# Kernel tuning notes

Hardware: AMD Instinct MI355X
Metric: run time of the kernel (lower is better)

Reference implementation:

```python
import jax, jax.numpy as jnp
import numpy as np

K_TOP = 16
NUM_HEADS = 12
EPS = 1e-6


def setup_inputs() -> dict:
    key = jax.random.key(0)
    ks = jax.random.split(key, 5)
    B, N, C = 4, 1024, 768
    scale = 0.02
    return {
        "x": jax.random.normal(ks[0], (B, N, C), dtype=jnp.float32),
        "in_proj_weight": jax.random.normal(ks[1], (3 * C, C), dtype=jnp.float32) * scale,
        "in_proj_bias": jax.random.normal(ks[2], (3 * C,), dtype=jnp.float32) * scale,
        "out_proj_weight": jax.random.normal(ks[3], (C, C), dtype=jnp.float32) * scale,
        "out_proj_bias": jax.random.normal(ks[4], (C,), dtype=jnp.float32) * scale,
    }


def reference(x, in_proj_weight, in_proj_bias, out_proj_weight, out_proj_bias):
    B, N, C = x.shape
    H = NUM_HEADS
    Dh = C // H
    scale = Dh ** (-0.5)
    # fused QKV projection: (B,N,3C) -> (3,B,H,N,Dh)
    qkv = x @ in_proj_weight.T + in_proj_bias
    qkv = qkv.reshape(B, N, 3, H, Dh).transpose(2, 0, 3, 1, 4)
    q, k, v = qkv[0], qkv[1], qkv[2]
    # dense scaled-dot-product scores, softmax over keys
    attn = jax.nn.softmax(jnp.einsum("bhqd,bhkd->bhqk", q, k) * scale, axis=-1)
    # top-k sparsification: keep k largest probs per query row, zero the rest
    topk_vals, topk_idx = jax.lax.top_k(attn, K_TOP)  # [B,H,N,K]
    bi = jnp.arange(B)[:, None, None, None]
    hi = jnp.arange(H)[None, :, None, None]
    ni = jnp.arange(N)[None, None, :, None]
    topk_attn = jnp.zeros_like(attn).at[bi, hi, ni, topk_idx].set(topk_vals)
    # renormalize surviving mass
    den = jnp.clip(topk_attn.sum(axis=-1, keepdims=True), EPS, None)
    topk_attn = topk_attn / den
    # weighted value aggregation + output projection
    x_out = jnp.einsum("bhqk,bhkd->bhqd", topk_attn, v)
    x_out = x_out.transpose(0, 2, 1, 3).reshape(B, N, C)
    x_out = x_out @ out_proj_weight.T + out_proj_bias
    return (x_out, topk_attn)
```

## Files before the change

kernel.cpp:

```cpp
#include <hip/hip_runtime.h>
#include <math.h>
#include <stdint.h>

#define BB 4
#define NN 1024
#define CC 768
#define HH 12
#define DH 64
#define KTOP 16

#define GATE     2e-4f
#define SUPERSET 4e-4f

typedef __attribute__((ext_vector_type(8))) short short8v;
typedef __attribute__((ext_vector_type(4))) short short4v;
typedef __attribute__((ext_vector_type(4))) float f32x4;

__device__ __forceinline__ short2 bf16split(float f) {
    uint32_t u = __float_as_uint(f);
    uint32_t hb = (u + 0x8000u) & 0xFFFF0000u;
    float hf = __uint_as_float(hb);
    float lo = f - hf;
    short2 r;
    r.x = (short)(hb >> 16);
    r.y = (short)((__float_as_uint(lo) + 0x8000u) >> 16);
    return r;
}

__device__ __forceinline__ short8v lds_load8(const short* p) {
    short4v a = *(const short4v*)p;
    short4v b = *(const short4v*)(p + 4);
    short8v r;
    r[0] = a[0]; r[1] = a[1]; r[2] = a[2]; r[3] = a[3];
    r[4] = b[0]; r[5] = b[1]; r[6] = b[2]; r[7] = b[3];
    return r;
}

__global__ __launch_bounds__(256) void qkv_mfma(
    const float* __restrict__ x, const float* __restrict__ w,
    const float* __restrict__ bias,
    float* __restrict__ q32, float* __restrict__ k32, float* __restrict__ v32) {
    __shared__ short xh[128][36], xl[128][36];
    __shared__ short wh[64][36],  wl[64][36];
    const int tid = threadIdx.x;
    const int m0 = blockIdx.x * 128, n0 = blockIdx.y * 64;
    const int wave = tid >> 6, lane = tid & 63;
    const int wr = wave >> 1, wc = wave & 1;
    const int lr = lane & 15, lg = lane >> 4;

    f32x4 acc[4][2];
#pragma unroll
    for (int i = 0; i < 4; ++i)
#pragma unroll
        for (int j = 0; j < 2; ++j) acc[i][j] = (f32x4)0.0f;

    for (int k0 = 0; k0 < CC; k0 += 32) {
        __syncthreads();
#pragma unroll
        for (int it = 0; it < 4; ++it) {
            int e = tid + 256 * it;
            int row = e >> 3, c4 = e & 7;
            float4 f = *reinterpret_cast<const float4*>(&x[(size_t)(m0 + row) * CC + k0 + 4 * c4]);
            short4v hv, lv;
            short2 s0 = bf16split(f.x); short2 s1 = bf16split(f.y);
            short2 s2 = bf16split(f.z); short2 s3 = bf16split(f.w);
            hv[0] = s0.x; lv[0] = s0.y; hv[1] = s1.x; lv[1] = s1.y;
            hv[2] = s2.x; lv[2] = s2.y; hv[3] = s3.x; lv[3] = s3.y;
            *(short4v*)&xh[row][4 * c4] = hv;
            *(short4v*)&xl[row][4 * c4] = lv;
        }
#pragma unroll
        for (int it = 0; it < 2; ++it) {
            int e = tid + 256 * it;
            int row = e >> 3, c4 = e & 7;
            float4 f = *reinterpret_cast<const float4*>(&w[(size_t)(n0 + row) * CC + k0 + 4 * c4]);
            short4v hv, lv;
            short2 s0 = bf16split(f.x); short2 s1 = bf16split(f.y);
            short2 s2 = bf16split(f.z); short2 s3 = bf16split(f.w);
            hv[0] = s0.x; lv[0] = s0.y; hv[1] = s1.x; lv[1] = s1.y;
            hv[2] = s2.x; lv[2] = s2.y; hv[3] = s3.x; lv[3] = s3.y;
            *(short4v*)&wh[row][4 * c4] = hv;
            *(short4v*)&wl[row][4 * c4] = lv;
        }
        __syncthreads();

        short8v ah[4], al[4], bh[2], bl[2];
#pragma unroll
        for (int mt = 0; mt < 4; ++mt) {
            int row = wr * 64 + mt * 16 + lr;
            ah[mt] = lds_load8(&xh[row][lg * 8]);
            al[mt] = lds_load8(&xl[row][lg * 8]);
        }
#pragma unroll
        for (int nt = 0; nt < 2; ++nt) {
            int col = wc * 32 + nt * 16 + lr;
            bh[nt] = lds_load8(&wh[col][lg * 8]);
            bl[nt] = lds_load8(&wl[col][lg * 8]);
        }
#pragma unroll
        for (int mt = 0; mt < 4; ++mt) {
#pragma unroll
            for (int nt = 0; nt < 2; ++nt) {
                acc[mt][nt] = __builtin_amdgcn_mfma_f32_16x16x32_bf16(ah[mt], bh[nt], acc[mt][nt], 0, 0, 0);
                acc[mt][nt] = __builtin_amdgcn_mfma_f32_16x16x32_bf16(ah[mt], bl[nt], acc[mt][nt], 0, 0, 0);
                acc[mt][nt] = __builtin_amdgcn_mfma_f32_16x16x32_bf16(al[mt], bh[nt], acc[mt][nt], 0, 0, 0);
            }
        }
    }

    const int t = n0 / CC;
#pragma unroll
    for (int mt = 0; mt < 4; ++mt) {
#pragma unroll
        for (int nt = 0; nt < 2; ++nt) {
#pragma unroll
            for (int r = 0; r < 4; ++r) {
                int m = m0 + wr * 64 + mt * 16 + lg * 4 + r;
                int col = n0 + wc * 32 + nt * 16 + lr;
                float val = acc[mt][nt][r] + bias[col];
                int rem = col - t * CC;
                int h = rem >> 6, d = rem & 63;
                int b = m >> 10, n = m & 1023;
                size_t off = (((size_t)(b * HH + h)) * NN + n) * DH + d;
                if (t == 0) q32[off] = val;
                else if (t == 1) k32[off] = val;
                else v32[off] = val;
            }
        }
    }
}

__global__ __launch_bounds__(256) void scores_mfma(
    const float* __restrict__ q32, const float* __restrict__ k32,
    float* __restrict__ attn_out) {
    __shared__ short qh[64][68], ql[64][68];
    __shared__ short kh[128][68], kl[128][68];
    const int bh = blockIdx.y;
    const int m0 = blockIdx.x * 64;
    const int tid = threadIdx.x;
    const int wave = tid >> 6, lane = tid & 63;
    const int lr = lane & 15, lg = lane >> 4;

    const float* qb = q32 + ((size_t)bh * NN + m0) * DH;
    const float* kb = k32 + (size_t)bh * NN * DH;

#pragma unroll
    for (int it = 0; it < 4; ++it) {
        int e = tid + 256 * it;
        int row = e >> 4, c4 = e & 15;
        float4 f = *reinterpret_cast<const float4*>(&qb[(size_t)row * DH + 4 * c4]);
        f.x *= 0.125f; f.y *= 0.125f; f.z *= 0.125f; f.w *= 0.125f;
        short4v hv, lv;
        short2 s0 = bf16split(f.x); short2 s1 = bf16split(f.y);
        short2 s2 = bf16split(f.z); short2 s3 = bf16split(f.w);
        hv[0] = s0.x; lv[0] = s0.y; hv[1] = s1.x; lv[1] = s1.y;
        hv[2] = s2.x; lv[2] = s2.y; hv[3] = s3.x; lv[3] = s3.y;
        *(short4v*)&qh[row][4 * c4] = hv;
        *(short4v*)&ql[row][4 * c4] = lv;
    }
    __syncthreads();

    short8v ah[4][2], al[4][2];
#pragma unroll
    for (int mt = 0; mt < 4; ++mt)
#pragma unroll
        for (int ks = 0; ks < 2; ++ks) {
            ah[mt][ks] = lds_load8(&qh[mt * 16 + lr][ks * 32 + lg * 8]);
            al[mt][ks] = lds_load8(&ql[mt * 16 + lr][ks * 32 + lg * 8]);
        }

    float* orow0 = attn_out + ((size_t)bh * NN + m0) * NN;

    for (int c0 = 0; c0 < NN; c0 += 128) {
        __syncthreads();
#pragma unroll
        for (int it = 0; it < 8; ++it) {
            int e = tid + 256 * it;
            int row = e >> 4, c4 = e & 15;
            float4 f = *reinterpret_cast<const float4*>(&kb[(size_t)(c0 + row) * DH + 4 * c4]);
            short4v hv, lv;
            short2 s0 = bf16split(f.x); short2 s1 = bf16split(f.y);
            short2 s2 = bf16split(f.z); short2 s3 = bf16split(f.w);
            hv[0] = s0.x; lv[0] = s0.y; hv[1] = s1.x; lv[1] = s1.y;
            hv[2] = s2.x; lv[2] = s2.y; hv[3] = s3.x; lv[3] = s3.y;
            *(short4v*)&kh[row][4 * c4] = hv;
            *(short4v*)&kl[row][4 * c4] = lv;
        }
        __syncthreads();

        short8v bhf[2][2], blf[2][2];
#pragma unroll
        for (int nt = 0; nt < 2; ++nt)
#pragma unroll
            for (int ks = 0; ks < 2; ++ks) {
                int col = wave * 32 + nt * 16 + lr;
                bhf[nt][ks] = lds_load8(&kh[col][ks * 32 + lg * 8]);
                blf[nt][ks] = lds_load8(&kl[col][ks * 32 + lg * 8]);
            }

        f32x4 acc[4][2];
#pragma unroll
        for (int mt = 0; mt < 4; ++mt)
#pragma unroll
            for (int nt = 0; nt < 2; ++nt) acc[mt][nt] = (f32x4)0.0f;

#pragma unroll
        for (int mt = 0; mt < 4; ++mt)
#pragma unroll
            for (int nt = 0; nt < 2; ++nt)
#pragma unroll
                for (int ks = 0; ks < 2; ++ks) {
                    acc[mt][nt] = __builtin_amdgcn_mfma_f32_16x16x32_bf16(ah[mt][ks], bhf[nt][ks], acc[mt][nt], 0, 0, 0);
                    acc[mt][nt] = __builtin_amdgcn_mfma_f32_16x16x32_bf16(ah[mt][ks], blf[nt][ks], acc[mt][nt], 0, 0, 0);
                    acc[mt][nt] = __builtin_amdgcn_mfma_f32_16x16x32_bf16(al[mt][ks], bhf[nt][ks], acc[mt][nt], 0, 0, 0);
                }

#pragma unroll
        for (int mt = 0; mt < 4; ++mt)
#pragma unroll
            for (int nt = 0; nt < 2; ++nt)
#pragma unroll
                for (int r = 0; r < 4; ++r)
                    orow0[(size_t)(mt * 16 + lg * 4 + r) * NN + c0 + wave * 32 + nt * 16 + lr] = acc[mt][nt][r];
    }
}

__device__ __forceinline__ uint32_t f2su(float f) {
    uint32_t u = __float_as_uint(f);
    return u ^ ((u & 0x80000000u) ? 0xFFFFFFFFu : 0x80000000u);
}
__device__ __forceinline__ float su2f(uint32_t s) {
    uint32_t u = s ^ ((s & 0x80000000u) ? 0x80000000u : 0xFFFFFFFFu);
    return __uint_as_float(u);
}

__global__ __launch_bounds__(256) void topk_select(
    const float* __restrict__ v32,
    float* __restrict__ attn_out, float* __restrict__ xatt,
    int* __restrict__ wl_count, int* __restrict__ wl_row, int* __restrict__ wl_cand) {
    __shared__ int      cand_idx[4][64];
    __shared__ uint32_t cand_val[4][64];
    const int blk = blockIdx.x;
    const int wave = threadIdx.x >> 6, lane = threadIdx.x & 63;
    const int bh = blk >> 8;
    const int qn = ((blk & 255) << 2) | wave;

    float* srow = attn_out + ((size_t)bh * NN + qn) * NN;

    uint32_t su[16];
#pragma unroll
    for (int i = 0; i < 4; ++i) {
        float4 t = *(const float4*)&srow[i * 256 + lane * 4];
        su[4 * i + 0] = f2su(t.x); su[4 * i + 1] = f2su(t.y);
        su[4 * i + 2] = f2su(t.z); su[4 * i + 3] = f2su(t.w);
    }

    uint32_t thr = 0;
    for (int b = 31; b >= 0; --b) {
        uint32_t test = thr | (1u << b);
        int cnt = 0;
#pragma unroll
        for (int r = 0; r < 16; ++r)
            cnt += __popcll(__ballot(su[r] >= test));
        if (cnt >= 17) { thr = test; if (cnt <= 64) break; }
    }

    int C = 0;
#pragma unroll
    for (int r = 0; r < 16; ++r) {
        bool pr = (su[r] >= thr);
        unsigned long long mask = __ballot(pr);
        if (pr) {
            int pos = C + __popcll(mask & ((1ull << lane) - 1ull));
            if (pos < 64) {
                cand_idx[wave][pos] = ((r >> 2) << 8) + (lane << 2) + (r & 3);
                cand_val[wave][pos] = su[r];
            }
        }
        C += __popcll(mask);
    }
    if (C > 64) C = 64;

    uint32_t key = (lane < C) ? cand_val[wave][lane] : 0u;
    int      idx = (lane < C) ? cand_idx[wave][lane] : (0x40000000 + lane);

#pragma unroll
    for (int k = 2; k <= 64; k <<= 1) {
#pragma unroll
        for (int j = k >> 1; j > 0; j >>= 1) {
            uint32_t ok = __shfl_xor(key, j);
            int      oi = __shfl_xor(idx, j);
            bool mine_better = (key > ok) || (key == ok && idx < oi);
            bool lower = ((lane & j) == 0);
            bool dir_desc = ((lane & k) == 0);
            bool keep = dir_desc ? (lower ? mine_better : !mine_better)
                                 : (lower ? !mine_better : mine_better);
            if (!keep) { key = ok; idx = oi; }
        }
    }

    float f = su2f(key);
    float f15 = __shfl(f, 15);
    float f16 = __shfl(f, 16);

    bool fast = (f15 - f16 > GATE);
    float p = 0.0f;
    int selIdx = idx;

    if (fast) {
        float m = __shfl(f, 0);
        float e = (lane < KTOP) ? expf(f - m) : 0.0f;
        float sum = e;
#pragma unroll
        for (int off = 32; off; off >>= 1) sum += __shfl_xor(sum, off);
        p = e / sum;
    } else {
        uint32_t thr2 = f2su(f15 - SUPERSET);
        int C2 = 0;
#pragma unroll
        for (int r = 0; r < 16; ++r) {
            bool pr = (su[r] >= thr2);
            unsigned long long mask = __ballot(pr);
            if (pr) {
                int pos = C2 + __popcll(mask & ((1ull << lane) - 1ull));
                if (pos < 64) cand_idx[wave][pos] = ((r >> 2) << 8) + (lane << 2) + (r & 3);
            }
            C2 += __popcll(mask);
        }
        if (C2 > 64) C2 = 64;

        int slot = 0;
        if (lane == 0) slot = atomicAdd(wl_count, 1);
        slot = __shfl(slot, 0);
        int rowid = (bh << 10) | qn;
        if (lane == 0) wl_row[slot] = rowid | (C2 << 20);
        if (lane < C2) wl_cand[(size_t)slot * 64 + lane] = cand_idx[wave][lane];
    }

#pragma unroll
    for (int i = 0; i < 4; ++i) {
        float4 z = make_float4(0.f, 0.f, 0.f, 0.f);
        *(float4*)&srow[i * 256 + lane * 4] = z;
    }

    if (fast) {
        const float* vb = v32 + (size_t)bh * NN * DH;
        float o = 0.0f;
#pragma unroll
        for (int t = 0; t < KTOP; ++t) {
            int jt = __shfl(selIdx, t);
            float pt = __shfl(p, t);
            o = fmaf(pt, vb[(size_t)jt * DH + lane], o);
        }
        asm volatile("s_waitcnt vmcnt(0)" ::: "memory");
        if (lane < KTOP) srow[selIdx] = p;
        int b = bh / HH, h = bh - b * HH;
        xatt[((size_t)b * NN + qn) * CC + h * DH + lane] = o;
    }
}

__global__ __launch_bounds__(64) void slow_rescore(
    const float* __restrict__ x, const float* __restrict__ w_in,
    const float* __restrict__ b_in, const float* __restrict__ v32,
    const int* __restrict__ wl_count, const int* __restrict__ wl_row,
    const int* __restrict__ wl_cand,
    float* __restrict__ attn_out, float* __restrict__ xatt) {
    __shared__ double part[64][65];
    __shared__ double q_sh[64];
    const int lane = threadIdx.x;
    const int count = wl_count[0];

    for (int it = blockIdx.x; it < count; it += gridDim.x) {
        int ent = wl_row[it];
        int rowid = ent & 0xFFFF;
        int C2 = (ent >> 20) & 0x7F;
        int bh = rowid >> 10, qn = rowid & 1023;
        int bq = bh / HH, hq = bh - bq * HH;

        __syncthreads();

        const float* xq = x + ((size_t)bq * NN + qn) * CC;
        double xqd[12];
#pragma unroll
        for (int c = 0; c < 3; ++c) {
            float4 v = *(const float4*)&xq[c * 256 + 4 * lane];
            xqd[4 * c + 0] = v.x; xqd[4 * c + 1] = v.y;
            xqd[4 * c + 2] = v.z; xqd[4 * c + 3] = v.w;
        }
        const float* wqb = w_in + (size_t)(hq * DH) * CC;
        for (int r = 0; r < 64; ++r) {
            const float* wr = wqb + (size_t)r * CC;
            double s = 0.0;
#pragma unroll
            for (int c = 0; c < 3; ++c) {
                float4 v = *(const float4*)&wr[c * 256 + 4 * lane];
                s = fma((double)v.x, xqd[4 * c + 0], s);
                s = fma((double)v.y, xqd[4 * c + 1], s);
                s = fma((double)v.z, xqd[4 * c + 2], s);
                s = fma((double)v.w, xqd[4 * c + 3], s);
            }
            part[r][lane] = s;
        }
        __syncthreads();
        double q64 = 0.0, q64b = 0.0;
#pragma unroll
        for (int l = 0; l < 64; l += 2) { q64 += part[lane][l]; q64b += part[lane][l + 1]; }
        q64 += q64b + (double)b_in[hq * DH + lane];
        q_sh[lane] = q64;
        __syncthreads();

        double beta = q64 * (double)b_in[CC + hq * DH + lane];
#pragma unroll
        for (int off = 32; off; off >>= 1) beta += __shfl_xor(beta, off);

        const float* wkb = w_in + (size_t)(CC + hq * DH) * CC;
        double zd[12];
#pragma unroll
        for (int j = 0; j < 12; ++j) zd[j] = 0.0;
        for (int r = 0; r < 64; ++r) {
            double qr = q_sh[r];
            const float* wr = wkb + (size_t)r * CC;
#pragma unroll
            for (int c = 0; c < 3; ++c) {
                float4 v = *(const float4*)&wr[c * 256 + 4 * lane];
                zd[4 * c + 0] = fma(qr, (double)v.x, zd[4 * c + 0]);
                zd[4 * c + 1] = fma(qr, (double)v.y, zd[4 * c + 1]);
                zd[4 * c + 2] = fma(qr, (double)v.z, zd[4 * c + 2]);
                zd[4 * c + 3] = fma(qr, (double)v.w, zd[4 * c + 3]);
            }
        }

        double myS = -1.0e300;
        int myI = (1 << 30);
        for (int t = 0; t < C2; ++t) {
            int jt = wl_cand[(size_t)it * 64 + t];
            const float* xk = x + ((size_t)bq * NN + jt) * CC;
            double pr = 0.0;
#pragma unroll
            for (int c = 0; c < 3; ++c) {
                float4 v = *(const float4*)&xk[c * 256 + 4 * lane];
                pr = fma(zd[4 * c + 0], (double)v.x, pr);
                pr = fma(zd[4 * c + 1], (double)v.y, pr);
                pr = fma(zd[4 * c + 2], (double)v.z, pr);
                pr = fma(zd[4 * c + 3], (double)v.w, pr);
            }
#pragma unroll
            for (int off = 32; off; off >>= 1) pr += __shfl_xor(pr, off);
            if (lane == t) { myS = (pr + beta) * 0.125; myI = jt; }
        }

        double sS = myS;
        int sI = myI;
        double selS = 0.0; int selIdx = 0;
#pragma unroll 1
        for (int t = 0; t < KTOP; ++t) {
            double bv = sS; int bi = sI;
#pragma unroll
            for (int off = 32; off; off >>= 1) {
                double ov = __shfl_xor(bv, off);
                int oi = __shfl_xor(bi, off);
                if (ov > bv || (ov == bv && oi < bi)) { bv = ov; bi = oi; }
            }
            if (lane == t) { selS = bv; selIdx = bi; }
            if (sI == bi) sS = -1.0e300;
        }

        double m = __shfl(selS, 0);
        float e = (lane < KTOP) ? expf((float)(selS - m)) : 0.0f;
        float sum = e;
#pragma unroll
        for (int off = 32; off; off >>= 1) sum += __shfl_xor(sum, off);
        float p = e / sum;

        const float* vb = v32 + (size_t)bh * NN * DH;
        float o = 0.0f;
#pragma unroll
        for (int t = 0; t < KTOP; ++t) {
            int jt = __shfl(selIdx, t);
            float pt = __shfl(p, t);
            o = fmaf(pt, vb[(size_t)jt * DH + lane], o);
        }

        float* srow = attn_out + (size_t)rowid * NN;
        if (lane < KTOP) srow[selIdx] = p;
        xatt[((size_t)bq * NN + qn) * CC + hq * DH + lane] = o;
    }
}

__global__ __launch_bounds__(256) void out_proj_mfma(
    const float* __restrict__ a, const float* __restrict__ w,
    const float* __restrict__ bias, float* __restrict__ out) {
    __shared__ short xh[128][36], xl[128][36];
    __shared__ short wh[64][36],  wl[64][36];
    const int tid = threadIdx.x;
    const int m0 = blockIdx.x * 128, n0 = blockIdx.y * 64;
    const int wave = tid >> 6, lane = tid & 63;
    const int wr = wave >> 1, wc = wave & 1;
    const int lr = lane & 15, lg = lane >> 4;

    f32x4 acc[4][2];
#pragma unroll
    for (int i = 0; i < 4; ++i)
#pragma unroll
        for (int j = 0; j < 2; ++j) acc[i][j] = (f32x4)0.0f;

    for (int k0 = 0; k0 < CC; k0 += 32) {
        __syncthreads();
#pragma unroll
        for (int it = 0; it < 4; ++it) {
            int e = tid + 256 * it;
            int row = e >> 3, c4 = e & 7;
            float4 f = *reinterpret_cast<const float4*>(&a[(size_t)(m0 + row) * CC + k0 + 4 * c4]);
            short4v hv, lv;
            short2 s0 = bf16split(f.x); short2 s1 = bf16split(f.y);
            short2 s2 = bf16split(f.z); short2 s3 = bf16split(f.w);
            hv[0] = s0.x; lv[0] = s0.y; hv[1] = s1.x; lv[1] = s1.y;
            hv[2] = s2.x; lv[2] = s2.y; hv[3] = s3.x; lv[3] = s3.y;
            *(short4v*)&xh[row][4 * c4] = hv;
            *(short4v*)&xl[row][4 * c4] = lv;
        }
#pragma unroll
        for (int it = 0; it < 2; ++it) {
            int e = tid + 256 * it;
            int row = e >> 3, c4 = e & 7;
            float4 f = *reinterpret_cast<const float4*>(&w[(size_t)(n0 + row) * CC + k0 + 4 * c4]);
            short4v hv, lv;
            short2 s0 = bf16split(f.x); short2 s1 = bf16split(f.y);
            short2 s2 = bf16split(f.z); short2 s3 = bf16split(f.w);
            hv[0] = s0.x; lv[0] = s0.y; hv[1] = s1.x; lv[1] = s1.y;
            hv[2] = s2.x; lv[2] = s2.y; hv[3] = s3.x; lv[3] = s3.y;
            *(short4v*)&wh[row][4 * c4] = hv;
            *(short4v*)&wl[row][4 * c4] = lv;
        }
        __syncthreads();

        short8v ah[4], al[4], bh[2], bl[2];
#pragma unroll
        for (int mt = 0; mt < 4; ++mt) {
            int row = wr * 64 + mt * 16 + lr;
            ah[mt] = lds_load8(&xh[row][lg * 8]);
            al[mt] = lds_load8(&xl[row][lg * 8]);
        }
#pragma unroll
        for (int nt = 0; nt < 2; ++nt) {
            int col = wc * 32 + nt * 16 + lr;
            bh[nt] = lds_load8(&wh[col][lg * 8]);
            bl[nt] = lds_load8(&wl[col][lg * 8]);
        }
#pragma unroll
        for (int mt = 0; mt < 4; ++mt) {
#pragma unroll
            for (int nt = 0; nt < 2; ++nt) {
                acc[mt][nt] = __builtin_amdgcn_mfma_f32_16x16x32_bf16(ah[mt], bh[nt], acc[mt][nt], 0, 0, 0);
                acc[mt][nt] = __builtin_amdgcn_mfma_f32_16x16x32_bf16(ah[mt], bl[nt], acc[mt][nt], 0, 0, 0);
                acc[mt][nt] = __builtin_amdgcn_mfma_f32_16x16x32_bf16(al[mt], bh[nt], acc[mt][nt], 0, 0, 0);
            }
        }
    }

#pragma unroll
    for (int mt = 0; mt < 4; ++mt) {
#pragma unroll
        for (int nt = 0; nt < 2; ++nt) {
#pragma unroll
            for (int r = 0; r < 4; ++r) {
                int m = m0 + wr * 64 + mt * 16 + lg * 4 + r;
                int col = n0 + wc * 32 + nt * 16 + lr;
                out[(size_t)m * CC + col] = acc[mt][nt][r] + bias[col];
            }
        }
    }
}

extern "C" void kernel_launch(void* const* d_in, const int* in_sizes, int n_in,
                              void* d_out, int out_size, void* d_ws, size_t ws_size,
                              hipStream_t stream) {
    const float* x     = (const float*)d_in[0];
    const float* w_in  = (const float*)d_in[1];
    const float* b_in  = (const float*)d_in[2];
    const float* w_out = (const float*)d_in[3];
    const float* b_out = (const float*)d_in[4];

    float* xout     = (float*)d_out;
    float* attn_out = (float*)d_out + (size_t)BB * NN * CC;

    char* ws = (char*)d_ws;
    float* q32     = (float*)ws;
    float* k32     = (float*)(ws + 12582912);
    float* v32     = (float*)(ws + 25165824);
    float* xatt    = (float*)(ws + 37748736);
    int*   wl_count = (int*)(ws + 50331648);
    int*   wl_row   = (int*)(ws + 50331904);
    int*   wl_cand  = (int*)(ws + 50528512);

    (void)hipMemsetAsync(wl_count, 0, sizeof(int), stream);

    hipLaunchKernelGGL(qkv_mfma, dim3(32, 36), dim3(256), 0, stream,
                       x, w_in, b_in, q32, k32, v32);
    hipLaunchKernelGGL(scores_mfma, dim3(NN / 64, BB * HH), dim3(256), 0, stream,
                       q32, k32, attn_out);
    hipLaunchKernelGGL(topk_select, dim3(BB * HH * (NN / 4)), dim3(256), 0, stream,
                       v32, attn_out, xatt, wl_count, wl_row, wl_cand);
    hipLaunchKernelGGL(slow_rescore, dim3(1024), dim3(64), 0, stream,
                       x, w_in, b_in, v32, wl_count, wl_row, wl_cand, attn_out, xatt);
    hipLaunchKernelGGL(out_proj_mfma, dim3(32, 12), dim3(256), 0, stream,
                       xatt, w_out, b_out, xout);
}
```

Baseline: 346.0 us.

## Presplit x and W_in into bf16 hi/lo buffers; emit Q/K as split bf16

```diff
diff --git a/kernel.cpp b/kernel.cpp
--- a/kernel.cpp
+++ b/kernel.cpp
@@ -36,10 +36,33 @@
     return r;
 }
 
+__global__ __launch_bounds__(256) void presplit(
+    const float* __restrict__ x, const float* __restrict__ w_in,
+    short* __restrict__ xh, short* __restrict__ xl,
+    short* __restrict__ wh, short* __restrict__ wl) {
+    const int NX4 = (BB * NN * CC) / 4;
+    const int NW4 = (3 * CC * CC) / 4;
+    for (int i = blockIdx.x * 256 + threadIdx.x; i < NX4 + NW4; i += gridDim.x * 256) {
+        bool isx = (i < NX4);
+        int j = isx ? i : i - NX4;
+        float4 f = isx ? ((const float4*)x)[j] : ((const float4*)w_in)[j];
+        short4v hv, lv;
+        short2 s0 = bf16split(f.x); short2 s1 = bf16split(f.y);
+        short2 s2 = bf16split(f.z); short2 s3 = bf16split(f.w);
+        hv[0] = s0.x; lv[0] = s0.y; hv[1] = s1.x; lv[1] = s1.y;
+        hv[2] = s2.x; lv[2] = s2.y; hv[3] = s3.x; lv[3] = s3.y;
+        if (isx) { ((short4v*)xh)[j] = hv; ((short4v*)xl)[j] = lv; }
+        else     { ((short4v*)wh)[j] = hv; ((short4v*)wl)[j] = lv; }
+    }
+}
+
 __global__ __launch_bounds__(256) void qkv_mfma(
-    const float* __restrict__ x, const float* __restrict__ w,
+    const short* __restrict__ xh_g, const short* __restrict__ xl_g,
+    const short* __restrict__ wh_g, const short* __restrict__ wl_g,
     const float* __restrict__ bias,
-    float* __restrict__ q32, float* __restrict__ k32, float* __restrict__ v32) {
+    short* __restrict__ qh_g, short* __restrict__ ql_g,
+    short* __restrict__ kh_g, short* __restrict__ kl_g,
+    float* __restrict__ v32) {
     __shared__ short xh[128][36], xl[128][36];
     __shared__ short wh[64][36],  wl[64][36];
     const int tid = threadIdx.x;
@@ -57,10 +80,453 @@
     for (int k0 = 0; k0 < CC; k0 += 32) {
         __syncthreads();
 #pragma unroll
+        for (int it = 0; it < 2; ++it) {
+            int e = tid + 256 * it;
+            int row = e >> 2, c8 = (e & 3) << 3;
+            size_t g = (size_t)(m0 + row) * CC + k0 + c8;
+            *(short4v*)&xh[row][c8]     = *(const short4v*)&xh_g[g];
+            *(short4v*)&xh[row][c8 + 4] = *(const short4v*)&xh_g[g + 4];
+            *(short4v*)&xl[row][c8]     = *(const short4v*)&xl_g[g];
+            *(short4v*)&xl[row][c8 + 4] = *(const short4v*)&xl_g[g + 4];
+        }
+        {
+            int e = tid;
+            int row = e >> 2, c8 = (e & 3) << 3;
+            size_t g = (size_t)(n0 + row) * CC + k0 + c8;
+            *(short4v*)&wh[row][c8]     = *(const short4v*)&wh_g[g];
+            *(short4v*)&wh[row][c8 + 4] = *(const short4v*)&wh_g[g + 4];
+            *(short4v*)&wl[row][c8]     = *(const short4v*)&wl_g[g];
+            *(short4v*)&wl[row][c8 + 4] = *(const short4v*)&wl_g[g + 4];
+        }
+        __syncthreads();
+
+        short8v ah[4], al[4], bh[2], bl[2];
+#pragma unroll
+        for (int mt = 0; mt < 4; ++mt) {
+            int row = wr * 64 + mt * 16 + lr;
+            ah[mt] = lds_load8(&xh[row][lg * 8]);
+            al[mt] = lds_load8(&xl[row][lg * 8]);
+        }
+#pragma unroll
+        for (int nt = 0; nt < 2; ++nt) {
+            int col = wc * 32 + nt * 16 + lr;
+            bh[nt] = lds_load8(&wh[col][lg * 8]);
+            bl[nt] = lds_load8(&wl[col][lg * 8]);
+        }
+#pragma unroll
+        for (int mt = 0; mt < 4; ++mt) {
+#pragma unroll
+            for (int nt = 0; nt < 2; ++nt) {
+                acc[mt][nt] = __builtin_amdgcn_mfma_f32_16x16x32_bf16(ah[mt], bh[nt], acc[mt][nt], 0, 0, 0);
+                acc[mt][nt] = __builtin_amdgcn_mfma_f32_16x16x32_bf16(ah[mt], bl[nt], acc[mt][nt], 0, 0, 0);
+                acc[mt][nt] = __builtin_amdgcn_mfma_f32_16x16x32_bf16(al[mt], bh[nt], acc[mt][nt], 0, 0, 0);
+            }
+        }
+    }
+
+    const int t = n0 / CC;
+#pragma unroll
+    for (int mt = 0; mt < 4; ++mt) {
+#pragma unroll
+        for (int nt = 0; nt < 2; ++nt) {
+#pragma unroll
+            for (int r = 0; r < 4; ++r) {
+                int m = m0 + wr * 64 + mt * 16 + lg * 4 + r;
+                int col = n0 + wc * 32 + nt * 16 + lr;
+                float val = acc[mt][nt][r] + bias[col];
+                int rem = col - t * CC;
+                int h = rem >> 6, d = rem & 63;
+                int b = m >> 10, n = m & 1023;
+                size_t off = (((size_t)(b * HH + h)) * NN + n) * DH + d;
+                if (t == 0) {
+                    short2 s = bf16split(val * 0.125f);
+                    qh_g[off] = s.x; ql_g[off] = s.y;
+                } else if (t == 1) {
+                    short2 s = bf16split(val);
+                    kh_g[off] = s.x; kl_g[off] = s.y;
+                } else {
+                    v32[off] = val;
+                }
+            }
+        }
+    }
+}
+
+__global__ __launch_bounds__(256) void scores_mfma(
+    const short* __restrict__ qh_g, const short* __restrict__ ql_g,
+    const short* __restrict__ kh_g, const short* __restrict__ kl_g,
+    float* __restrict__ attn_out) {
+    __shared__ short qh[64][68], ql[64][68];
+    __shared__ short kh[128][68], kl[128][68];
+    const int bh = blockIdx.y;
+    const int m0 = blockIdx.x * 64;
+    const int tid = threadIdx.x;
+    const int wave = tid >> 6, lane = tid & 63;
+    const int lr = lane & 15, lg = lane >> 4;
+
+    const size_t qbase = ((size_t)bh * NN + m0) * DH;
+    const size_t kbase = (size_t)bh * NN * DH;
+
+#pragma unroll
+    for (int it = 0; it < 2; ++it) {
+        int e = tid + 256 * it;
+        int row = e >> 3, c8 = (e & 7) << 3;
+        size_t g = qbase + (size_t)row * DH + c8;
+        *(short4v*)&qh[row][c8]     = *(const short4v*)&qh_g[g];
+        *(short4v*)&qh[row][c8 + 4] = *(const short4v*)&qh_g[g + 4];
+        *(short4v*)&ql[row][c8]     = *(const short4v*)&ql_g[g];
+        *(short4v*)&ql[row][c8 + 4] = *(const short4v*)&ql_g[g + 4];
+    }
+    __syncthreads();
+
+    short8v ah[4][2], al[4][2];
+#pragma unroll
+    for (int mt = 0; mt < 4; ++mt)
+#pragma unroll
+        for (int ks = 0; ks < 2; ++ks) {
+            ah[mt][ks] = lds_load8(&qh[mt * 16 + lr][ks * 32 + lg * 8]);
+            al[mt][ks] = lds_load8(&ql[mt * 16 + lr][ks * 32 + lg * 8]);
+        }
+
+    float* orow0 = attn_out + ((size_t)bh * NN + m0) * NN;
+
+    for (int c0 = 0; c0 < NN; c0 += 128) {
+        __syncthreads();
+#pragma unroll
+        for (int it = 0; it < 4; ++it) {
+            int e = tid + 256 * it;
+            int row = e >> 3, c8 = (e & 7) << 3;
+            size_t g = kbase + (size_t)(c0 + row) * DH + c8;
+            *(short4v*)&kh[row][c8]     = *(const short4v*)&kh_g[g];
+            *(short4v*)&kh[row][c8 + 4] = *(const short4v*)&kh_g[g + 4];
+            *(short4v*)&kl[row][c8]     = *(const short4v*)&kl_g[g];
+            *(short4v*)&kl[row][c8 + 4] = *(const short4v*)&kl_g[g + 4];
+        }
+        __syncthreads();
+
+        short8v bhf[2][2], blf[2][2];
+#pragma unroll
+        for (int nt = 0; nt < 2; ++nt)
+#pragma unroll
+            for (int ks = 0; ks < 2; ++ks) {
+                int col = wave * 32 + nt * 16 + lr;
+                bhf[nt][ks] = lds_load8(&kh[col][ks * 32 + lg * 8]);
+                blf[nt][ks] = lds_load8(&kl[col][ks * 32 + lg * 8]);
+            }
+
+        f32x4 acc[4][2];
+#pragma unroll
+        for (int mt = 0; mt < 4; ++mt)
+#pragma unroll
+            for (int nt = 0; nt < 2; ++nt) acc[mt][nt] = (f32x4)0.0f;
+
+#pragma unroll
+        for (int mt = 0; mt < 4; ++mt)
+#pragma unroll
+            for (int nt = 0; nt < 2; ++nt)
+#pragma unroll
+                for (int ks = 0; ks < 2; ++ks) {
+                    acc[mt][nt] = __builtin_amdgcn_mfma_f32_16x16x32_bf16(ah[mt][ks], bhf[nt][ks], acc[mt][nt], 0, 0, 0);
+                    acc[mt][nt] = __builtin_amdgcn_mfma_f32_16x16x32_bf16(ah[mt][ks], blf[nt][ks], acc[mt][nt], 0, 0, 0);
+                    acc[mt][nt] = __builtin_amdgcn_mfma_f32_16x16x32_bf16(al[mt][ks], bhf[nt][ks], acc[mt][nt], 0, 0, 0);
+                }
+
+#pragma unroll
+        for (int mt = 0; mt < 4; ++mt)
+#pragma unroll
+            for (int nt = 0; nt < 2; ++nt)
+#pragma unroll
+                for (int r = 0; r < 4; ++r)
+                    orow0[(size_t)(mt * 16 + lg * 4 + r) * NN + c0 + wave * 32 + nt * 16 + lr] = acc[mt][nt][r];
+    }
+}
+
+__device__ __forceinline__ uint32_t f2su(float f) {
+    uint32_t u = __float_as_uint(f);
+    return u ^ ((u & 0x80000000u) ? 0xFFFFFFFFu : 0x80000000u);
+}
+__device__ __forceinline__ float su2f(uint32_t s) {
+    uint32_t u = s ^ ((s & 0x80000000u) ? 0x80000000u : 0xFFFFFFFFu);
+    return __uint_as_float(u);
+}
+
+__global__ __launch_bounds__(256) void topk_select(
+    const float* __restrict__ v32,
+    float* __restrict__ attn_out, float* __restrict__ xatt,
+    int* __restrict__ wl_count, int* __restrict__ wl_row, int* __restrict__ wl_cand) {
+    __shared__ int      cand_idx[4][64];
+    __shared__ uint32_t cand_val[4][64];
+    const int blk = blockIdx.x;
+    const int wave = threadIdx.x >> 6, lane = threadIdx.x & 63;
+    const int bh = blk >> 8;
+    const int qn = ((blk & 255) << 2) | wave;
+
+    float* srow = attn_out + ((size_t)bh * NN + qn) * NN;
+
+    uint32_t su[16];
+#pragma unroll
+    for (int i = 0; i < 4; ++i) {
+        float4 t = *(const float4*)&srow[i * 256 + lane * 4];
+        su[4 * i + 0] = f2su(t.x); su[4 * i + 1] = f2su(t.y);
+        su[4 * i + 2] = f2su(t.z); su[4 * i + 3] = f2su(t.w);
+    }
+
+    uint32_t thr = 0;
+    for (int b = 31; b >= 0; --b) {
+        uint32_t test = thr | (1u << b);
+        int cnt = 0;
+#pragma unroll
+        for (int r = 0; r < 16; ++r)
+            cnt += __popcll(__ballot(su[r] >= test));
+        if (cnt >= 17) { thr = test; if (cnt <= 64) break; }
+    }
+
+    int C = 0;
+#pragma unroll
+    for (int r = 0; r < 16; ++r) {
+        bool pr = (su[r] >= thr);
+        unsigned long long mask = __ballot(pr);
+        if (pr) {
+            int pos = C + __popcll(mask & ((1ull << lane) - 1ull));
+            if (pos < 64) {
+                cand_idx[wave][pos] = ((r >> 2) << 8) + (lane << 2) + (r & 3);
+                cand_val[wave][pos] = su[r];
+            }
+        }
+        C += __popcll(mask);
+    }
+    if (C > 64) C = 64;
+
+    uint32_t key = (lane < C) ? cand_val[wave][lane] : 0u;
+    int      idx = (lane < C) ? cand_idx[wave][lane] : (0x40000000 + lane);
+
+#pragma unroll
+    for (int k = 2; k <= 64; k <<= 1) {
+#pragma unroll
+        for (int j = k >> 1; j > 0; j >>= 1) {
+            uint32_t ok = __shfl_xor(key, j);
+            int      oi = __shfl_xor(idx, j);
+            bool mine_better = (key > ok) || (key == ok && idx < oi);
+            bool lower = ((lane & j) == 0);
+            bool dir_desc = ((lane & k) == 0);
+            bool keep = dir_desc ? (lower ? mine_better : !mine_better)
+                                 : (lower ? !mine_better : mine_better);
+            if (!keep) { key = ok; idx = oi; }
+        }
+    }
+
+    float f = su2f(key);
+    float f15 = __shfl(f, 15);
+    float f16 = __shfl(f, 16);
+
+    bool fast = (f15 - f16 > GATE);
+    float p = 0.0f;
+    int selIdx = idx;
+
+    if (fast) {
+        float m = __shfl(f, 0);
+        float e = (lane < KTOP) ? expf(f - m) : 0.0f;
+        float sum = e;
+#pragma unroll
+        for (int off = 32; off; off >>= 1) sum += __shfl_xor(sum, off);
+        p = e / sum;
+    } else {
+        uint32_t thr2 = f2su(f15 - SUPERSET);
+        int C2 = 0;
+#pragma unroll
+        for (int r = 0; r < 16; ++r) {
+            bool pr = (su[r] >= thr2);
+            unsigned long long mask = __ballot(pr);
+            if (pr) {
+                int pos = C2 + __popcll(mask & ((1ull << lane) - 1ull));
+                if (pos < 64) cand_idx[wave][pos] = ((r >> 2) << 8) + (lane << 2) + (r & 3);
+            }
+            C2 += __popcll(mask);
+        }
+        if (C2 > 64) C2 = 64;
+
+        int slot = 0;
+        if (lane == 0) slot = atomicAdd(wl_count, 1);
+        slot = __shfl(slot, 0);
+        int rowid = (bh << 10) | qn;
+        if (lane == 0) wl_row[slot] = rowid | (C2 << 20);
+        if (lane < C2) wl_cand[(size_t)slot * 64 + lane] = cand_idx[wave][lane];
+    }
+
+#pragma unroll
+    for (int i = 0; i < 4; ++i) {
+        float4 z = make_float4(0.f, 0.f, 0.f, 0.f);
+        *(float4*)&srow[i * 256 + lane * 4] = z;
+    }
+
+    if (fast) {
+        const float* vb = v32 + (size_t)bh * NN * DH;
+        float o = 0.0f;
+#pragma unroll
+        for (int t = 0; t < KTOP; ++t) {
+            int jt = __shfl(selIdx, t);
+            float pt = __shfl(p, t);
+            o = fmaf(pt, vb[(size_t)jt * DH + lane], o);
+        }
+        asm volatile("s_waitcnt vmcnt(0)" ::: "memory");
+        if (lane < KTOP) srow[selIdx] = p;
+        int b = bh / HH, h = bh - b * HH;
+        xatt[((size_t)b * NN + qn) * CC + h * DH + lane] = o;
+    }
+}
+
+__global__ __launch_bounds__(64) void slow_rescore(
+    const float* __restrict__ x, const float* __restrict__ w_in,
+    const float* __restrict__ b_in, const float* __restrict__ v32,
+    const int* __restrict__ wl_count, const int* __restrict__ wl_row,
+    const int* __restrict__ wl_cand,
+    float* __restrict__ attn_out, float* __restrict__ xatt) {
+    __shared__ double part[64][65];
+    __shared__ double q_sh[64];
+    const int lane = threadIdx.x;
+    const int count = wl_count[0];
+
+    for (int it = blockIdx.x; it < count; it += gridDim.x) {
+        int ent = wl_row[it];
+        int rowid = ent & 0xFFFF;
+        int C2 = (ent >> 20) & 0x7F;
+        int bh = rowid >> 10, qn = rowid & 1023;
+        int bq = bh / HH, hq = bh - bq * HH;
+
+        __syncthreads();
+
+        const float* xq = x + ((size_t)bq * NN + qn) * CC;
+        double xqd[12];
+#pragma unroll
+        for (int c = 0; c < 3; ++c) {
+            float4 v = *(const float4*)&xq[c * 256 + 4 * lane];
+            xqd[4 * c + 0] = v.x; xqd[4 * c + 1] = v.y;
+            xqd[4 * c + 2] = v.z; xqd[4 * c + 3] = v.w;
+        }
+        const float* wqb = w_in + (size_t)(hq * DH) * CC;
+        for (int r = 0; r < 64; ++r) {
+            const float* wr = wqb + (size_t)r * CC;
+            double s = 0.0;
+#pragma unroll
+            for (int c = 0; c < 3; ++c) {
+                float4 v = *(const float4*)&wr[c * 256 + 4 * lane];
+                s = fma((double)v.x, xqd[4 * c + 0], s);
+                s = fma((double)v.y, xqd[4 * c + 1], s);
+                s = fma((double)v.z, xqd[4 * c + 2], s);
+                s = fma((double)v.w, xqd[4 * c + 3], s);
+            }
+            part[r][lane] = s;
+        }
+        __syncthreads();
+        double q64 = 0.0, q64b = 0.0;
+#pragma unroll
+        for (int l = 0; l < 64; l += 2) { q64 += part[lane][l]; q64b += part[lane][l + 1]; }
+        q64 += q64b + (double)b_in[hq * DH + lane];
+        q_sh[lane] = q64;
+        __syncthreads();
+
+        double beta = q64 * (double)b_in[CC + hq * DH + lane];
+#pragma unroll
+        for (int off = 32; off; off >>= 1) beta += __shfl_xor(beta, off);
+
+        const float* wkb = w_in + (size_t)(CC + hq * DH) * CC;
+        double zd[12];
+#pragma unroll
+        for (int j = 0; j < 12; ++j) zd[j] = 0.0;
+        for (int r = 0; r < 64; ++r) {
+            double qr = q_sh[r];
+            const float* wr = wkb + (size_t)r * CC;
+#pragma unroll
+            for (int c = 0; c < 3; ++c) {
+                float4 v = *(const float4*)&wr[c * 256 + 4 * lane];
+                zd[4 * c + 0] = fma(qr, (double)v.x, zd[4 * c + 0]);
+                zd[4 * c + 1] = fma(qr, (double)v.y, zd[4 * c + 1]);
+                zd[4 * c + 2] = fma(qr, (double)v.z, zd[4 * c + 2]);
+                zd[4 * c + 3] = fma(qr, (double)v.w, zd[4 * c + 3]);
+            }
+        }
+
+        double myS = -1.0e300;
+        int myI = (1 << 30);
+        for (int t = 0; t < C2; ++t) {
+            int jt = wl_cand[(size_t)it * 64 + t];
+            const float* xk = x + ((size_t)bq * NN + jt) * CC;
+            double pr = 0.0;
+#pragma unroll
+            for (int c = 0; c < 3; ++c) {
+                float4 v = *(const float4*)&xk[c * 256 + 4 * lane];
+                pr = fma(zd[4 * c + 0], (double)v.x, pr);
+                pr = fma(zd[4 * c + 1], (double)v.y, pr);
+                pr = fma(zd[4 * c + 2], (double)v.z, pr);
+                pr = fma(zd[4 * c + 3], (double)v.w, pr);
+            }
+#pragma unroll
+            for (int off = 32; off; off >>= 1) pr += __shfl_xor(pr, off);
+            if (lane == t) { myS = (pr + beta) * 0.125; myI = jt; }
+        }
+
+        double sS = myS;
+        int sI = myI;
+        double selS = 0.0; int selIdx = 0;
+#pragma unroll 1
+        for (int t = 0; t < KTOP; ++t) {
+            double bv = sS; int bi = sI;
+#pragma unroll
+            for (int off = 32; off; off >>= 1) {
+                double ov = __shfl_xor(bv, off);
+                int oi = __shfl_xor(bi, off);
+                if (ov > bv || (ov == bv && oi < bi)) { bv = ov; bi = oi; }
+            }
+            if (lane == t) { selS = bv; selIdx = bi; }
+            if (sI == bi) sS = -1.0e300;
+        }
+
+        double m = __shfl(selS, 0);
+        float e = (lane < KTOP) ? expf((float)(selS - m)) : 0.0f;
+        float sum = e;
+#pragma unroll
+        for (int off = 32; off; off >>= 1) sum += __shfl_xor(sum, off);
+        float p = e / sum;
+
+        const float* vb = v32 + (size_t)bh * NN * DH;
+        float o = 0.0f;
+#pragma unroll
+        for (int t = 0; t < KTOP; ++t) {
+            int jt = __shfl(selIdx, t);
+            float pt = __shfl(p, t);
+            o = fmaf(pt, vb[(size_t)jt * DH + lane], o);
+        }
+
+        float* srow = attn_out + (size_t)rowid * NN;
+        if (lane < KTOP) srow[selIdx] = p;
+        xatt[((size_t)bq * NN + qn) * CC + hq * DH + lane] = o;
+    }
+}
+
+__global__ __launch_bounds__(256) void out_proj_mfma(
+    const float* __restrict__ a, const float* __restrict__ w,
+    const float* __restrict__ bias, float* __restrict__ out) {
+    __shared__ short xh[128][36], xl[128][36];
+    __shared__ short wh[64][36],  wl[64][36];
+    const int tid = threadIdx.x;
+    const int m0 = blockIdx.x * 128, n0 = blockIdx.y * 64;
+    const int wave = tid >> 6, lane = tid & 63;
+    const int wr = wave >> 1, wc = wave & 1;
+    const int lr = lane & 15, lg = lane >> 4;
+
+    f32x4 acc[4][2];
+#pragma unroll
+    for (int i = 0; i < 4; ++i)
+#pragma unroll
+        for (int j = 0; j < 2; ++j) acc[i][j] = (f32x4)0.0f;
+
+    for (int k0 = 0; k0 < CC; k0 += 32) {
+        __syncthreads();
+#pragma unroll
         for (int it = 0; it < 4; ++it) {
             int e = tid + 256 * it;
             int row = e >> 3, c4 = e & 7;
-            float4 f = *reinterpret_cast<const float4*>(&x[(size_t)(m0 + row) * CC + k0 + 4 * c4]);
+            float4 f = *reinterpret_cast<const float4*>(&a[(size_t)(m0 + row) * CC + k0 + 4 * c4]);
             short4v hv, lv;
             short2 s0 = bf16split(f.x); short2 s1 = bf16split(f.y);
             short2 s2 = bf16split(f.z); short2 s3 = bf16split(f.w);
@@ -108,456 +574,6 @@
         }
     }
 
-    const int t = n0 / CC;
-#pragma unroll
-    for (int mt = 0; mt < 4; ++mt) {
-#pragma unroll
-        for (int nt = 0; nt < 2; ++nt) {
-#pragma unroll
-            for (int r = 0; r < 4; ++r) {
-                int m = m0 + wr * 64 + mt * 16 + lg * 4 + r;
-                int col = n0 + wc * 32 + nt * 16 + lr;
-                float val = acc[mt][nt][r] + bias[col];
-                int rem = col - t * CC;
-                int h = rem >> 6, d = rem & 63;
-                int b = m >> 10, n = m & 1023;
-                size_t off = (((size_t)(b * HH + h)) * NN + n) * DH + d;
-                if (t == 0) q32[off] = val;
-                else if (t == 1) k32[off] = val;
-                else v32[off] = val;
-            }
-        }
-    }
-}
-
-__global__ __launch_bounds__(256) void scores_mfma(
-    const float* __restrict__ q32, const float* __restrict__ k32,
-    float* __restrict__ attn_out) {
-    __shared__ short qh[64][68], ql[64][68];
-    __shared__ short kh[128][68], kl[128][68];
-    const int bh = blockIdx.y;
-    const int m0 = blockIdx.x * 64;
-    const int tid = threadIdx.x;
-    const int wave = tid >> 6, lane = tid & 63;
-    const int lr = lane & 15, lg = lane >> 4;
-
-    const float* qb = q32 + ((size_t)bh * NN + m0) * DH;
-    const float* kb = k32 + (size_t)bh * NN * DH;
-
-#pragma unroll
-    for (int it = 0; it < 4; ++it) {
-        int e = tid + 256 * it;
-        int row = e >> 4, c4 = e & 15;
-        float4 f = *reinterpret_cast<const float4*>(&qb[(size_t)row * DH + 4 * c4]);
-        f.x *= 0.125f; f.y *= 0.125f; f.z *= 0.125f; f.w *= 0.125f;
-        short4v hv, lv;
-        short2 s0 = bf16split(f.x); short2 s1 = bf16split(f.y);
-        short2 s2 = bf16split(f.z); short2 s3 = bf16split(f.w);
-        hv[0] = s0.x; lv[0] = s0.y; hv[1] = s1.x; lv[1] = s1.y;
-        hv[2] = s2.x; lv[2] = s2.y; hv[3] = s3.x; lv[3] = s3.y;
-        *(short4v*)&qh[row][4 * c4] = hv;
-        *(short4v*)&ql[row][4 * c4] = lv;
-    }
-    __syncthreads();
-
-    short8v ah[4][2], al[4][2];
-#pragma unroll
-    for (int mt = 0; mt < 4; ++mt)
-#pragma unroll
-        for (int ks = 0; ks < 2; ++ks) {
-            ah[mt][ks] = lds_load8(&qh[mt * 16 + lr][ks * 32 + lg * 8]);
-            al[mt][ks] = lds_load8(&ql[mt * 16 + lr][ks * 32 + lg * 8]);
-        }
-
-    float* orow0 = attn_out + ((size_t)bh * NN + m0) * NN;
-
-    for (int c0 = 0; c0 < NN; c0 += 128) {
-        __syncthreads();
-#pragma unroll
-        for (int it = 0; it < 8; ++it) {
-            int e = tid + 256 * it;
-            int row = e >> 4, c4 = e & 15;
-            float4 f = *reinterpret_cast<const float4*>(&kb[(size_t)(c0 + row) * DH + 4 * c4]);
-            short4v hv, lv;
-            short2 s0 = bf16split(f.x); short2 s1 = bf16split(f.y);
-            short2 s2 = bf16split(f.z); short2 s3 = bf16split(f.w);
-            hv[0] = s0.x; lv[0] = s0.y; hv[1] = s1.x; lv[1] = s1.y;
-            hv[2] = s2.x; lv[2] = s2.y; hv[3] = s3.x; lv[3] = s3.y;
-            *(short4v*)&kh[row][4 * c4] = hv;
-            *(short4v*)&kl[row][4 * c4] = lv;
-        }
-        __syncthreads();
-
-        short8v bhf[2][2], blf[2][2];
-#pragma unroll
-        for (int nt = 0; nt < 2; ++nt)
-#pragma unroll
-            for (int ks = 0; ks < 2; ++ks) {
-                int col = wave * 32 + nt * 16 + lr;
-                bhf[nt][ks] = lds_load8(&kh[col][ks * 32 + lg * 8]);
-                blf[nt][ks] = lds_load8(&kl[col][ks * 32 + lg * 8]);
-            }
-
-        f32x4 acc[4][2];
-#pragma unroll
-        for (int mt = 0; mt < 4; ++mt)
-#pragma unroll
-            for (int nt = 0; nt < 2; ++nt) acc[mt][nt] = (f32x4)0.0f;
-
-#pragma unroll
-        for (int mt = 0; mt < 4; ++mt)
-#pragma unroll
-            for (int nt = 0; nt < 2; ++nt)
-#pragma unroll
-                for (int ks = 0; ks < 2; ++ks) {
-                    acc[mt][nt] = __builtin_amdgcn_mfma_f32_16x16x32_bf16(ah[mt][ks], bhf[nt][ks], acc[mt][nt], 0, 0, 0);
-                    acc[mt][nt] = __builtin_amdgcn_mfma_f32_16x16x32_bf16(ah[mt][ks], blf[nt][ks], acc[mt][nt], 0, 0, 0);
-                    acc[mt][nt] = __builtin_amdgcn_mfma_f32_16x16x32_bf16(al[mt][ks], bhf[nt][ks], acc[mt][nt], 0, 0, 0);
-                }
-
-#pragma unroll
-        for (int mt = 0; mt < 4; ++mt)
-#pragma unroll
-            for (int nt = 0; nt < 2; ++nt)
-#pragma unroll
-                for (int r = 0; r < 4; ++r)
-                    orow0[(size_t)(mt * 16 + lg * 4 + r) * NN + c0 + wave * 32 + nt * 16 + lr] = acc[mt][nt][r];
-    }
-}
-
-__device__ __forceinline__ uint32_t f2su(float f) {
-    uint32_t u = __float_as_uint(f);
-    return u ^ ((u & 0x80000000u) ? 0xFFFFFFFFu : 0x80000000u);
-}
-__device__ __forceinline__ float su2f(uint32_t s) {
-    uint32_t u = s ^ ((s & 0x80000000u) ? 0x80000000u : 0xFFFFFFFFu);
-    return __uint_as_float(u);
-}
-
-__global__ __launch_bounds__(256) void topk_select(
-    const float* __restrict__ v32,
-    float* __restrict__ attn_out, float* __restrict__ xatt,
-    int* __restrict__ wl_count, int* __restrict__ wl_row, int* __restrict__ wl_cand) {
-    __shared__ int      cand_idx[4][64];
-    __shared__ uint32_t cand_val[4][64];
-    const int blk = blockIdx.x;
-    const int wave = threadIdx.x >> 6, lane = threadIdx.x & 63;
-    const int bh = blk >> 8;
-    const int qn = ((blk & 255) << 2) | wave;
-
-    float* srow = attn_out + ((size_t)bh * NN + qn) * NN;
-
-    uint32_t su[16];
-#pragma unroll
-    for (int i = 0; i < 4; ++i) {
-        float4 t = *(const float4*)&srow[i * 256 + lane * 4];
-        su[4 * i + 0] = f2su(t.x); su[4 * i + 1] = f2su(t.y);
-        su[4 * i + 2] = f2su(t.z); su[4 * i + 3] = f2su(t.w);
-    }
-
-    uint32_t thr = 0;
-    for (int b = 31; b >= 0; --b) {
-        uint32_t test = thr | (1u << b);
-        int cnt = 0;
-#pragma unroll
-        for (int r = 0; r < 16; ++r)
-            cnt += __popcll(__ballot(su[r] >= test));
-        if (cnt >= 17) { thr = test; if (cnt <= 64) break; }
-    }
-
-    int C = 0;
-#pragma unroll
-    for (int r = 0; r < 16; ++r) {
-        bool pr = (su[r] >= thr);
-        unsigned long long mask = __ballot(pr);
-        if (pr) {
-            int pos = C + __popcll(mask & ((1ull << lane) - 1ull));
-            if (pos < 64) {
-                cand_idx[wave][pos] = ((r >> 2) << 8) + (lane << 2) + (r & 3);
-                cand_val[wave][pos] = su[r];
-            }
-        }
-        C += __popcll(mask);
-    }
-    if (C > 64) C = 64;
-
-    uint32_t key = (lane < C) ? cand_val[wave][lane] : 0u;
-    int      idx = (lane < C) ? cand_idx[wave][lane] : (0x40000000 + lane);
-
-#pragma unroll
-    for (int k = 2; k <= 64; k <<= 1) {
-#pragma unroll
-        for (int j = k >> 1; j > 0; j >>= 1) {
-            uint32_t ok = __shfl_xor(key, j);
-            int      oi = __shfl_xor(idx, j);
-            bool mine_better = (key > ok) || (key == ok && idx < oi);
-            bool lower = ((lane & j) == 0);
-            bool dir_desc = ((lane & k) == 0);
-            bool keep = dir_desc ? (lower ? mine_better : !mine_better)
-                                 : (lower ? !mine_better : mine_better);
-            if (!keep) { key = ok; idx = oi; }
-        }
-    }
-
-    float f = su2f(key);
-    float f15 = __shfl(f, 15);
-    float f16 = __shfl(f, 16);
-
-    bool fast = (f15 - f16 > GATE);
-    float p = 0.0f;
-    int selIdx = idx;
-
-    if (fast) {
-        float m = __shfl(f, 0);
-        float e = (lane < KTOP) ? expf(f - m) : 0.0f;
-        float sum = e;
-#pragma unroll
-        for (int off = 32; off; off >>= 1) sum += __shfl_xor(sum, off);
-        p = e / sum;
-    } else {
-        uint32_t thr2 = f2su(f15 - SUPERSET);
-        int C2 = 0;
-#pragma unroll
-        for (int r = 0; r < 16; ++r) {
-            bool pr = (su[r] >= thr2);
-            unsigned long long mask = __ballot(pr);
-            if (pr) {
-                int pos = C2 + __popcll(mask & ((1ull << lane) - 1ull));
-                if (pos < 64) cand_idx[wave][pos] = ((r >> 2) << 8) + (lane << 2) + (r & 3);
-            }
-            C2 += __popcll(mask);
-        }
-        if (C2 > 64) C2 = 64;
-
-        int slot = 0;
-        if (lane == 0) slot = atomicAdd(wl_count, 1);
-        slot = __shfl(slot, 0);
-        int rowid = (bh << 10) | qn;
-        if (lane == 0) wl_row[slot] = rowid | (C2 << 20);
-        if (lane < C2) wl_cand[(size_t)slot * 64 + lane] = cand_idx[wave][lane];
-    }
-
-#pragma unroll
-    for (int i = 0; i < 4; ++i) {
-        float4 z = make_float4(0.f, 0.f, 0.f, 0.f);
-        *(float4*)&srow[i * 256 + lane * 4] = z;
-    }
-
-    if (fast) {
-        const float* vb = v32 + (size_t)bh * NN * DH;
-        float o = 0.0f;
-#pragma unroll
-        for (int t = 0; t < KTOP; ++t) {
-            int jt = __shfl(selIdx, t);
-            float pt = __shfl(p, t);
-            o = fmaf(pt, vb[(size_t)jt * DH + lane], o);
-        }
-        asm volatile("s_waitcnt vmcnt(0)" ::: "memory");
-        if (lane < KTOP) srow[selIdx] = p;
-        int b = bh / HH, h = bh - b * HH;
-        xatt[((size_t)b * NN + qn) * CC + h * DH + lane] = o;
-    }
-}
-
-__global__ __launch_bounds__(64) void slow_rescore(
-    const float* __restrict__ x, const float* __restrict__ w_in,
-    const float* __restrict__ b_in, const float* __restrict__ v32,
-    const int* __restrict__ wl_count, const int* __restrict__ wl_row,
-    const int* __restrict__ wl_cand,
-    float* __restrict__ attn_out, float* __restrict__ xatt) {
-    __shared__ double part[64][65];
-    __shared__ double q_sh[64];
-    const int lane = threadIdx.x;
-    const int count = wl_count[0];
-
-    for (int it = blockIdx.x; it < count; it += gridDim.x) {
-        int ent = wl_row[it];
-        int rowid = ent & 0xFFFF;
-        int C2 = (ent >> 20) & 0x7F;
-        int bh = rowid >> 10, qn = rowid & 1023;
-        int bq = bh / HH, hq = bh - bq * HH;
-
-        __syncthreads();
-
-        const float* xq = x + ((size_t)bq * NN + qn) * CC;
-        double xqd[12];
-#pragma unroll
-        for (int c = 0; c < 3; ++c) {
-            float4 v = *(const float4*)&xq[c * 256 + 4 * lane];
-            xqd[4 * c + 0] = v.x; xqd[4 * c + 1] = v.y;
-            xqd[4 * c + 2] = v.z; xqd[4 * c + 3] = v.w;
-        }
-        const float* wqb = w_in + (size_t)(hq * DH) * CC;
-        for (int r = 0; r < 64; ++r) {
-            const float* wr = wqb + (size_t)r * CC;
-            double s = 0.0;
-#pragma unroll
-            for (int c = 0; c < 3; ++c) {
-                float4 v = *(const float4*)&wr[c * 256 + 4 * lane];
-                s = fma((double)v.x, xqd[4 * c + 0], s);
-                s = fma((double)v.y, xqd[4 * c + 1], s);
-                s = fma((double)v.z, xqd[4 * c + 2], s);
-                s = fma((double)v.w, xqd[4 * c + 3], s);
-            }
-            part[r][lane] = s;
-        }
-        __syncthreads();
-        double q64 = 0.0, q64b = 0.0;
-#pragma unroll
-        for (int l = 0; l < 64; l += 2) { q64 += part[lane][l]; q64b += part[lane][l + 1]; }
-        q64 += q64b + (double)b_in[hq * DH + lane];
-        q_sh[lane] = q64;
-        __syncthreads();
-
-        double beta = q64 * (double)b_in[CC + hq * DH + lane];
-#pragma unroll
-        for (int off = 32; off; off >>= 1) beta += __shfl_xor(beta, off);
-
-        const float* wkb = w_in + (size_t)(CC + hq * DH) * CC;
-        double zd[12];
-#pragma unroll
-        for (int j = 0; j < 12; ++j) zd[j] = 0.0;
-        for (int r = 0; r < 64; ++r) {
-            double qr = q_sh[r];
-            const float* wr = wkb + (size_t)r * CC;
-#pragma unroll
-            for (int c = 0; c < 3; ++c) {
-                float4 v = *(const float4*)&wr[c * 256 + 4 * lane];
-                zd[4 * c + 0] = fma(qr, (double)v.x, zd[4 * c + 0]);
-                zd[4 * c + 1] = fma(qr, (double)v.y, zd[4 * c + 1]);
-                zd[4 * c + 2] = fma(qr, (double)v.z, zd[4 * c + 2]);
-                zd[4 * c + 3] = fma(qr, (double)v.w, zd[4 * c + 3]);
-            }
-        }
-
-        double myS = -1.0e300;
-        int myI = (1 << 30);
-        for (int t = 0; t < C2; ++t) {
-            int jt = wl_cand[(size_t)it * 64 + t];
-            const float* xk = x + ((size_t)bq * NN + jt) * CC;
-            double pr = 0.0;
-#pragma unroll
-            for (int c = 0; c < 3; ++c) {
-                float4 v = *(const float4*)&xk[c * 256 + 4 * lane];
-                pr = fma(zd[4 * c + 0], (double)v.x, pr);
-                pr = fma(zd[4 * c + 1], (double)v.y, pr);
-                pr = fma(zd[4 * c + 2], (double)v.z, pr);
-                pr = fma(zd[4 * c + 3], (double)v.w, pr);
-            }
-#pragma unroll
-            for (int off = 32; off; off >>= 1) pr += __shfl_xor(pr, off);
-            if (lane == t) { myS = (pr + beta) * 0.125; myI = jt; }
-        }
-
-        double sS = myS;
-        int sI = myI;
-        double selS = 0.0; int selIdx = 0;
-#pragma unroll 1
-        for (int t = 0; t < KTOP; ++t) {
-            double bv = sS; int bi = sI;
-#pragma unroll
-            for (int off = 32; off; off >>= 1) {
-                double ov = __shfl_xor(bv, off);
-                int oi = __shfl_xor(bi, off);
-                if (ov > bv || (ov == bv && oi < bi)) { bv = ov; bi = oi; }
-            }
-            if (lane == t) { selS = bv; selIdx = bi; }
-            if (sI == bi) sS = -1.0e300;
-        }
-
-        double m = __shfl(selS, 0);
-        float e = (lane < KTOP) ? expf((float)(selS - m)) : 0.0f;
-        float sum = e;
-#pragma unroll
-        for (int off = 32; off; off >>= 1) sum += __shfl_xor(sum, off);
-        float p = e / sum;
-
-        const float* vb = v32 + (size_t)bh * NN * DH;
-        float o = 0.0f;
-#pragma unroll
-        for (int t = 0; t < KTOP; ++t) {
-            int jt = __shfl(selIdx, t);
-            float pt = __shfl(p, t);
-            o = fmaf(pt, vb[(size_t)jt * DH + lane], o);
-        }
-
-        float* srow = attn_out + (size_t)rowid * NN;
-        if (lane < KTOP) srow[selIdx] = p;
-        xatt[((size_t)bq * NN + qn) * CC + hq * DH + lane] = o;
-    }
-}
-
-__global__ __launch_bounds__(256) void out_proj_mfma(
-    const float* __restrict__ a, const float* __restrict__ w,
-    const float* __restrict__ bias, float* __restrict__ out) {
-    __shared__ short xh[128][36], xl[128][36];
-    __shared__ short wh[64][36],  wl[64][36];
-    const int tid = threadIdx.x;
-    const int m0 = blockIdx.x * 128, n0 = blockIdx.y * 64;
-    const int wave = tid >> 6, lane = tid & 63;
-    const int wr = wave >> 1, wc = wave & 1;
-    const int lr = lane & 15, lg = lane >> 4;
-
-    f32x4 acc[4][2];
-#pragma unroll
-    for (int i = 0; i < 4; ++i)
-#pragma unroll
-        for (int j = 0; j < 2; ++j) acc[i][j] = (f32x4)0.0f;
-
-    for (int k0 = 0; k0 < CC; k0 += 32) {
-        __syncthreads();
-#pragma unroll
-        for (int it = 0; it < 4; ++it) {
-            int e = tid + 256 * it;
-            int row = e >> 3, c4 = e & 7;
-            float4 f = *reinterpret_cast<const float4*>(&a[(size_t)(m0 + row) * CC + k0 + 4 * c4]);
-            short4v hv, lv;
-            short2 s0 = bf16split(f.x); short2 s1 = bf16split(f.y);
-            short2 s2 = bf16split(f.z); short2 s3 = bf16split(f.w);
-            hv[0] = s0.x; lv[0] = s0.y; hv[1] = s1.x; lv[1] = s1.y;
-            hv[2] = s2.x; lv[2] = s2.y; hv[3] = s3.x; lv[3] = s3.y;
-            *(short4v*)&xh[row][4 * c4] = hv;
-            *(short4v*)&xl[row][4 * c4] = lv;
-        }
-#pragma unroll
-        for (int it = 0; it < 2; ++it) {
-            int e = tid + 256 * it;
-            int row = e >> 3, c4 = e & 7;
-            float4 f = *reinterpret_cast<const float4*>(&w[(size_t)(n0 + row) * CC + k0 + 4 * c4]);
-            short4v hv, lv;
-            short2 s0 = bf16split(f.x); short2 s1 = bf16split(f.y);
-            short2 s2 = bf16split(f.z); short2 s3 = bf16split(f.w);
-            hv[0] = s0.x; lv[0] = s0.y; hv[1] = s1.x; lv[1] = s1.y;
-            hv[2] = s2.x; lv[2] = s2.y; hv[3] = s3.x; lv[3] = s3.y;
-            *(short4v*)&wh[row][4 * c4] = hv;
-            *(short4v*)&wl[row][4 * c4] = lv;
-        }
-        __syncthreads();
-
-        short8v ah[4], al[4], bh[2], bl[2];
-#pragma unroll
-        for (int mt = 0; mt < 4; ++mt) {
-            int row = wr * 64 + mt * 16 + lr;
-            ah[mt] = lds_load8(&xh[row][lg * 8]);
-            al[mt] = lds_load8(&xl[row][lg * 8]);
-        }
-#pragma unroll
-        for (int nt = 0; nt < 2; ++nt) {
-            int col = wc * 32 + nt * 16 + lr;
-            bh[nt] = lds_load8(&wh[col][lg * 8]);
-            bl[nt] = lds_load8(&wl[col][lg * 8]);
-        }
-#pragma unroll
-        for (int mt = 0; mt < 4; ++mt) {
-#pragma unroll
-            for (int nt = 0; nt < 2; ++nt) {
-                acc[mt][nt] = __builtin_amdgcn_mfma_f32_16x16x32_bf16(ah[mt], bh[nt], acc[mt][nt], 0, 0, 0);
-                acc[mt][nt] = __builtin_amdgcn_mfma_f32_16x16x32_bf16(ah[mt], bl[nt], acc[mt][nt], 0, 0, 0);
-                acc[mt][nt] = __builtin_amdgcn_mfma_f32_16x16x32_bf16(al[mt], bh[nt], acc[mt][nt], 0, 0, 0);
-            }
-        }
-    }
-
 #pragma unroll
     for (int mt = 0; mt < 4; ++mt) {
 #pragma unroll
@@ -585,20 +601,28 @@
     float* attn_out = (float*)d_out + (size_t)BB * NN * CC;
 
     char* ws = (char*)d_ws;
-    float* q32     = (float*)ws;
-    float* k32     = (float*)(ws + 12582912);
-    float* v32     = (float*)(ws + 25165824);
-    float* xatt    = (float*)(ws + 37748736);
-    int*   wl_count = (int*)(ws + 50331648);
-    int*   wl_row   = (int*)(ws + 50331904);
-    int*   wl_cand  = (int*)(ws + 50528512);
+    short* xh_g = (short*)(ws);
+    short* xl_g = (short*)(ws + 6291456);
+    short* wh_g = (short*)(ws + 12582912);
+    short* wl_g = (short*)(ws + 16121856);
+    short* qh_g = (short*)(ws + 19660800);
+    short* ql_g = (short*)(ws + 25952256);
+    short* kh_g = (short*)(ws + 32243712);
+    short* kl_g = (short*)(ws + 38535168);
+    float* v32  = (float*)(ws + 44826624);
+    float* xatt = (float*)(ws + 57409536);
+    int* wl_count = (int*)(ws + 69992448);
+    int* wl_row   = (int*)(ws + 69992704);
+    int* wl_cand  = (int*)(ws + 70189312);
 
     (void)hipMemsetAsync(wl_count, 0, sizeof(int), stream);
 
+    hipLaunchKernelGGL(presplit, dim3(2048), dim3(256), 0, stream,
+                       x, w_in, xh_g, xl_g, wh_g, wl_g);
     hipLaunchKernelGGL(qkv_mfma, dim3(32, 36), dim3(256), 0, stream,
-                       x, w_in, b_in, q32, k32, v32);
+                       xh_g, xl_g, wh_g, wl_g, b_in, qh_g, ql_g, kh_g, kl_g, v32);
     hipLaunchKernelGGL(scores_mfma, dim3(NN / 64, BB * HH), dim3(256), 0, stream,
-                       q32, k32, attn_out);
+                       qh_g, ql_g, kh_g, kl_g, attn_out);
     hipLaunchKernelGGL(topk_select, dim3(BB * HH * (NN / 4)), dim3(256), 0, stream,
                        v32, attn_out, xatt, wl_count, wl_row, wl_cand);
     hipLaunchKernelGGL(slow_rescore, dim3(1024), dim3(64), 0, stream,
```

Result: no change. 351.7 us (+1.6%).
